# Performance work log

Measured on AMD Instinct MI355X. Metric: run time of the kernel, lower is better.

The kernel has to match this reference:

```python
import jax, jax.numpy as jnp
import numpy as np

B = 32768
IN_DIM = 768
HIDDENS = [2048, 1024, 512]
EMBED_DIM = 128
NUM_EMB = 1024
DEPTH = 3


def setup_inputs() -> dict:
    key = jax.random.key(0)
    ks = jax.random.split(key, 20)
    d = {"x": jax.random.normal(ks[0], (B, IN_DIM), dtype=jnp.float32)}
    # Encoder: in -> h0 -> h1 -> h2 -> embed  (weights stored as [in, out])
    enc_dims = [IN_DIM] + HIDDENS + [EMBED_DIM]
    for i in range(4):
        fan_in = enc_dims[i]
        d[f"enc_W{i+1}"] = jax.random.normal(ks[1 + i], (enc_dims[i], enc_dims[i + 1]), dtype=jnp.float32) / np.sqrt(fan_in)
        d[f"enc_b{i+1}"] = jnp.zeros((enc_dims[i + 1],), dtype=jnp.float32)
    # Decoder: embed -> h0 -> h1 -> h2 -> in
    dec_dims = [EMBED_DIM] + HIDDENS + [IN_DIM]
    for i in range(4):
        fan_in = dec_dims[i]
        d[f"dec_W{i+1}"] = jax.random.normal(ks[5 + i], (dec_dims[i], dec_dims[i + 1]), dtype=jnp.float32) / np.sqrt(fan_in)
        d[f"dec_b{i+1}"] = jnp.zeros((dec_dims[i + 1],), dtype=jnp.float32)
    # Codebook (nn.Embedding weight, initialized ~ N(0,1) as in the module)
    d["codebook"] = jax.random.normal(ks[9], (NUM_EMB, EMBED_DIM), dtype=jnp.float32)
    return d


def _encoder(x, W1, b1, W2, b2, W3, b3, W4, b4):
    x = jax.nn.relu(x @ W1 + b1)
    x = jax.nn.relu(x @ W2 + b2)
    x = jax.nn.relu(x @ W3 + b3)
    return x @ W4 + b4


def _decoder(x, W1, b1, W2, b2, W3, b3, W4, b4):
    x = jax.nn.relu(x @ W1 + b1)
    x = jax.nn.relu(x @ W2 + b2)
    x = jax.nn.relu(x @ W3 + b3)
    return x @ W4 + b4


def reference(x,
              enc_W1, enc_b1, enc_W2, enc_b2, enc_W3, enc_b3, enc_W4, enc_b4,
              dec_W1, dec_b1, dec_W2, dec_b2, dec_W3, dec_b3, dec_W4, dec_b4,
              codebook):
    z = _encoder(x, enc_W1, enc_b1, enc_W2, enc_b2, enc_W3, enc_b3, enc_W4, enc_b4)
    z_det = jax.lax.stop_gradient(z)

    cb_sq = jnp.sum(codebook * codebook, axis=1)  # [K]
    residue = z_det
    z_hat = jnp.zeros_like(z_det)
    codes = []
    for _ in range(DEPTH):  # residual quantization loop
        # squared L2 distances [B, K]
        dist = (jnp.sum(residue * residue, axis=1, keepdims=True)
                + cb_sq
                - 2.0 * residue @ codebook.T)
        idx = jnp.argmin(dist, axis=1)          # [B]
        codes.append(idx)
        z_hat = z_hat + codebook[idx]           # gather codebook vectors
        residue = z_det - z_hat
    all_codes = jnp.stack(codes, axis=1)        # [B, DEPTH] int

    # straight-through estimator: forward uses z_hat, grad flows through z
    z_flow = z + jax.lax.stop_gradient(z_hat - z)
    x_recon = _decoder(z_flow, dec_W1, dec_b1, dec_W2, dec_b2, dec_W3, dec_b3, dec_W4, dec_b4)
    return (x_recon, all_codes)
```

## Files before the change

kernel.cpp:

```cpp
#include <hip/hip_runtime.h>

#define FLT_MAX_C 3.402823466e+38f

typedef __attribute__((ext_vector_type(8))) __bf16 bf16x8;
typedef __attribute__((ext_vector_type(4))) float f32x4;

static __device__ __forceinline__ ushort f2bf(float x) {
    union { float f; unsigned u; } v; v.f = x;
    unsigned r = (v.u + 0x7FFFu + ((v.u >> 16) & 1u)) >> 16;
    return (ushort)r;
}

static __device__ __forceinline__ void xcd_swz(int& bx, int& by) {
    const int gx = gridDim.x;
    const int nwg = gx * gridDim.y;
    const int bid = blockIdx.y * gx + blockIdx.x;
    const int q = nwg >> 3, r = nwg & 7;
    const int xcd = bid & 7, lid = bid >> 3;
    const int swz = (xcd < r ? xcd * (q + 1) : r * (q + 1) + (xcd - r) * q) + lid;
    bx = swz % gx;
    by = swz / gx;
}

template<bool RELU>
__device__ __forceinline__ void gemm_f32_dev(
    const float* __restrict__ A, const float* __restrict__ W,
    const float* __restrict__ bias, float* __restrict__ C, int K, int N,
    int bxi, int byi)
{
    __shared__ float As[8][128];
    __shared__ float Bs[8][132];
    const int tid = threadIdx.x;
    const int bm = byi << 7;
    const int bn = bxi << 7;

    const int la_row = tid >> 1;
    const int la_k   = (tid & 1) << 2;
    const int lb_row = tid >> 5;
    const int lb_col = (tid & 31) << 2;
    const int tm4 = (tid >> 4) << 2;
    const int tn4 = (tid & 15) << 2;

    float acc[8][8];
    #pragma unroll
    for (int i = 0; i < 8; ++i)
        #pragma unroll
        for (int j = 0; j < 8; ++j) acc[i][j] = 0.f;

    const float* aptr = A + (size_t)(bm + la_row) * K + la_k;
    const float* bptr = W + (size_t)lb_row * N + bn + lb_col;

    float4 av = *(const float4*)(aptr);
    float4 bv = *(const float4*)(bptr);

    for (int k0 = 0; k0 < K; k0 += 8) {
        __syncthreads();
        As[la_k + 0][la_row] = av.x;
        As[la_k + 1][la_row] = av.y;
        As[la_k + 2][la_row] = av.z;
        As[la_k + 3][la_row] = av.w;
        *(float4*)(&Bs[lb_row][lb_col]) = bv;
        __syncthreads();
        if (k0 + 8 < K) {
            av = *(const float4*)(aptr + k0 + 8);
            bv = *(const float4*)(bptr + (size_t)(k0 + 8) * N);
        }
        #pragma unroll
        for (int kk = 0; kk < 8; ++kk) {
            float a[8], b[8];
            *(float4*)(a)     = *(const float4*)(&As[kk][tm4]);
            *(float4*)(a + 4) = *(const float4*)(&As[kk][tm4 + 64]);
            *(float4*)(b)     = *(const float4*)(&Bs[kk][tn4]);
            *(float4*)(b + 4) = *(const float4*)(&Bs[kk][tn4 + 64]);
            #pragma unroll
            for (int i = 0; i < 8; ++i)
                #pragma unroll
                for (int j = 0; j < 8; ++j)
                    acc[i][j] = fmaf(a[i], b[j], acc[i][j]);
        }
    }

    float bv0[8];
    #pragma unroll
    for (int j = 0; j < 8; ++j)
        bv0[j] = bias[bn + tn4 + (j < 4 ? j : 60 + j)];

    #pragma unroll
    for (int i = 0; i < 8; ++i) {
        int row = bm + tm4 + (i < 4 ? i : 60 + i);
        float* cp = C + (size_t)row * N + bn + tn4;
        float4 v0, v1;
        v0.x = acc[i][0] + bv0[0]; v0.y = acc[i][1] + bv0[1];
        v0.z = acc[i][2] + bv0[2]; v0.w = acc[i][3] + bv0[3];
        v1.x = acc[i][4] + bv0[4]; v1.y = acc[i][5] + bv0[5];
        v1.z = acc[i][6] + bv0[6]; v1.w = acc[i][7] + bv0[7];
        if (RELU) {
            v0.x = fmaxf(v0.x, 0.f); v0.y = fmaxf(v0.y, 0.f);
            v0.z = fmaxf(v0.z, 0.f); v0.w = fmaxf(v0.w, 0.f);
            v1.x = fmaxf(v1.x, 0.f); v1.y = fmaxf(v1.y, 0.f);
            v1.z = fmaxf(v1.z, 0.f); v1.w = fmaxf(v1.w, 0.f);
        }
        *(float4*)(cp) = v0;
        *(float4*)(cp + 64) = v1;
    }
}

template<bool RELU>
__device__ __forceinline__ void gemm_f32_wide_dev(
    const float* __restrict__ A, const float* __restrict__ W,
    const float* __restrict__ bias, float* __restrict__ C, int K, int N,
    int bxi, int byi, void* smem)
{
    float (*As)[128] = (float(*)[128])smem;
    float (*Bs)[260] = (float(*)[260])((char*)smem + 4096);
    const int tid = threadIdx.x;
    const int bm = byi << 7;
    const int bn = bxi << 8;

    const int la_row = tid >> 1;
    const int la_k   = (tid & 1) << 2;
    const int tm4 = (tid >> 4) << 2;
    const int tn4 = (tid & 15) << 2;
    const int bf_row  = tid >> 6;
    const int bf_col4 = (tid & 63) << 2;

    float acc[8][16];
    #pragma unroll
    for (int i = 0; i < 8; ++i)
        #pragma unroll
        for (int j = 0; j < 16; ++j) acc[i][j] = 0.f;

    const float* aptr = A + (size_t)(bm + la_row) * K + la_k;
    const float* bptr = W + (size_t)bf_row * N + bn + bf_col4;

    float4 av = *(const float4*)(aptr);
    float4 bv0 = *(const float4*)(bptr);
    float4 bv1 = *(const float4*)(bptr + (size_t)4 * N);

    for (int k0 = 0; k0 < K; k0 += 8) {
        __syncthreads();
        As[la_k + 0][la_row] = av.x;
        As[la_k + 1][la_row] = av.y;
        As[la_k + 2][la_row] = av.z;
        As[la_k + 3][la_row] = av.w;
        *(float4*)(&Bs[bf_row][bf_col4])     = bv0;
        *(float4*)(&Bs[bf_row + 4][bf_col4]) = bv1;
        __syncthreads();
        if (k0 + 8 < K) {
            av  = *(const float4*)(aptr + k0 + 8);
            bv0 = *(const float4*)(bptr + (size_t)(k0 + 8) * N);
            bv1 = *(const float4*)(bptr + (size_t)(k0 + 12) * N);
        }
        #pragma unroll
        for (int kk = 0; kk < 8; ++kk) {
            float a[8], b[16];
            *(float4*)(a)      = *(const float4*)(&As[kk][tm4]);
            *(float4*)(a + 4)  = *(const float4*)(&As[kk][tm4 + 64]);
            #pragma unroll
            for (int q = 0; q < 4; ++q)
                *(float4*)(b + q * 4) = *(const float4*)(&Bs[kk][tn4 + 64 * q]);
            #pragma unroll
            for (int i = 0; i < 8; ++i)
                #pragma unroll
                for (int j = 0; j < 16; ++j)
                    acc[i][j] = fmaf(a[i], b[j], acc[i][j]);
        }
    }

    float bb[16];
    #pragma unroll
    for (int q = 0; q < 4; ++q)
        #pragma unroll
        for (int jj = 0; jj < 4; ++jj)
            bb[q * 4 + jj] = bias[bn + tn4 + 64 * q + jj];

    #pragma unroll
    for (int i = 0; i < 8; ++i) {
        int row = bm + tm4 + (i < 4 ? i : 60 + i);
        float* cp = C + (size_t)row * N + bn + tn4;
        #pragma unroll
        for (int q = 0; q < 4; ++q) {
            float4 v;
            v.x = acc[i][q * 4 + 0] + bb[q * 4 + 0];
            v.y = acc[i][q * 4 + 1] + bb[q * 4 + 1];
            v.z = acc[i][q * 4 + 2] + bb[q * 4 + 2];
            v.w = acc[i][q * 4 + 3] + bb[q * 4 + 3];
            if (RELU) {
                v.x = fmaxf(v.x, 0.f); v.y = fmaxf(v.y, 0.f);
                v.z = fmaxf(v.z, 0.f); v.w = fmaxf(v.w, 0.f);
            }
            *(float4*)(cp + 64 * q) = v;
        }
    }
}

template<bool RELU>
__device__ __forceinline__ void gemm_f32_64_dev(
    const float* __restrict__ A, const float* __restrict__ W,
    const float* __restrict__ bias, float* __restrict__ C, int K, int N,
    int bxi, int byi)
{
    __shared__ float As[16][64];
    __shared__ float Bs[16][132];
    const int tid = threadIdx.x;
    const int bm = byi << 6;
    const int bn = bxi << 7;

    const int la_row = tid & 63;
    const int la_k   = (tid >> 6) << 2;
    const int lb_row = tid >> 5;
    const int lb_col = (tid & 31) << 2;
    const int tr = tid >> 4;
    const int tc = tid & 15;

    float acc[4][8];
    #pragma unroll
    for (int i = 0; i < 4; ++i)
        #pragma unroll
        for (int j = 0; j < 8; ++j) acc[i][j] = 0.f;

    const float* aptr = A + (size_t)(bm + la_row) * K + la_k;
    const float* bptr = W + (size_t)lb_row * N + bn + lb_col;

    float4 av = *(const float4*)(aptr);
    float4 bv0 = *(const float4*)(bptr);
    float4 bv1 = *(const float4*)(bptr + (size_t)8 * N);

    for (int k0 = 0; k0 < K; k0 += 16) {
        __syncthreads();
        As[la_k + 0][la_row] = av.x;
        As[la_k + 1][la_row] = av.y;
        As[la_k + 2][la_row] = av.z;
        As[la_k + 3][la_row] = av.w;
        *(float4*)(&Bs[lb_row][lb_col]) = bv0;
        *(float4*)(&Bs[lb_row + 8][lb_col]) = bv1;
        __syncthreads();
        if (k0 + 16 < K) {
            av  = *(const float4*)(aptr + k0 + 16);
            bv0 = *(const float4*)(bptr + (size_t)(k0 + 16) * N);
            bv1 = *(const float4*)(bptr + (size_t)(k0 + 24) * N);
        }
        #pragma unroll
        for (int kk = 0; kk < 16; ++kk) {
            float a[4], b[8];
            *(float4*)(a) = *(const float4*)(&As[kk][tr << 2]);
            *(float4*)(b)     = *(const float4*)(&Bs[kk][tc << 2]);
            *(float4*)(b + 4) = *(const float4*)(&Bs[kk][(tc << 2) + 64]);
            #pragma unroll
            for (int i = 0; i < 4; ++i)
                #pragma unroll
                for (int j = 0; j < 8; ++j)
                    acc[i][j] = fmaf(a[i], b[j], acc[i][j]);
        }
    }

    float bb[8];
    #pragma unroll
    for (int j = 0; j < 8; ++j)
        bb[j] = bias[bn + (tc << 2) + (j < 4 ? j : 60 + j)];

    #pragma unroll
    for (int i = 0; i < 4; ++i) {
        float* cp = C + (size_t)(bm + (tr << 2) + i) * N + bn + (tc << 2);
        float4 v0, v1;
        v0.x = acc[i][0] + bb[0]; v0.y = acc[i][1] + bb[1];
        v0.z = acc[i][2] + bb[2]; v0.w = acc[i][3] + bb[3];
        v1.x = acc[i][4] + bb[4]; v1.y = acc[i][5] + bb[5];
        v1.z = acc[i][6] + bb[6]; v1.w = acc[i][7] + bb[7];
        if (RELU) {
            v0.x = fmaxf(v0.x, 0.f); v0.y = fmaxf(v0.y, 0.f);
            v0.z = fmaxf(v0.z, 0.f); v0.w = fmaxf(v0.w, 0.f);
            v1.x = fmaxf(v1.x, 0.f); v1.y = fmaxf(v1.y, 0.f);
            v1.z = fmaxf(v1.z, 0.f); v1.w = fmaxf(v1.w, 0.f);
        }
        *(float4*)(cp) = v0;
        *(float4*)(cp + 64) = v1;
    }
}

template<bool RELU, bool OUTF32>
__device__ __forceinline__ void gemm_bf16_dev(
    const ushort* __restrict__ A, const ushort* __restrict__ Wt,
    const float* __restrict__ bias, void* __restrict__ C, int K, int N,
    int bxi, int byi)
{
    __shared__ __align__(16) ushort As[128][64];
    __shared__ __align__(16) ushort Bs[128][64];
    const int tid  = threadIdx.x;
    const int lane = tid & 63;
    const int wv   = tid >> 6;
    const int wm   = (wv >> 1) << 6;
    const int wn   = (wv & 1) << 6;
    const int bm   = byi << 7;
    const int bn   = bxi << 7;
    const int lr   = lane & 15;
    const int lh   = lane >> 4;

    f32x4 acc[4][4];
    #pragma unroll
    for (int m = 0; m < 4; ++m)
        #pragma unroll
        for (int n = 0; n < 4; ++n) acc[m][n] = (f32x4){0.f, 0.f, 0.f, 0.f};

    for (int k0 = 0; k0 < K; k0 += 64) {
        __syncthreads();
        #pragma unroll
        for (int i = 0; i < 4; ++i) {
            const int c    = wv * 4 + i;
            const int boff = c * 1024 + lane * 16;
            const int r    = boff >> 7;
            const int cbt  = boff & 127;
            const char* sa = (const char*)A  + (((size_t)(bm + r) * K + k0) << 1) + cbt;
            const char* sb = (const char*)Wt + (((size_t)(bn + r) * K + k0) << 1) + cbt;
            __builtin_amdgcn_global_load_lds((const void*)sa, (void*)(&As[0][0] + c * 512), 16, 0, 0);
            __builtin_amdgcn_global_load_lds((const void*)sb, (void*)(&Bs[0][0] + c * 512), 16, 0, 0);
        }
        __syncthreads();
        #pragma unroll
        for (int kk = 0; kk < 64; kk += 32) {
            bf16x8 af[4], bfr[4];
            #pragma unroll
            for (int m = 0; m < 4; ++m)
                af[m] = *(const bf16x8*)&As[wm + m * 16 + lr][kk + lh * 8];
            #pragma unroll
            for (int n = 0; n < 4; ++n)
                bfr[n] = *(const bf16x8*)&Bs[wn + n * 16 + lr][kk + lh * 8];
            #pragma unroll
            for (int m = 0; m < 4; ++m)
                #pragma unroll
                for (int n = 0; n < 4; ++n)
                    acc[m][n] = __builtin_amdgcn_mfma_f32_16x16x32_bf16(
                        af[m], bfr[n], acc[m][n], 0, 0, 0);
        }
    }

    #pragma unroll
    for (int n = 0; n < 4; ++n) {
        const int col = bn + wn + n * 16 + lr;
        const float bcol = bias[col];
        #pragma unroll
        for (int m = 0; m < 4; ++m) {
            #pragma unroll
            for (int i = 0; i < 4; ++i) {
                const int row = bm + wm + m * 16 + lh * 4 + i;
                float v = acc[m][n][i] + bcol;
                if (RELU) v = fmaxf(v, 0.f);
                if (OUTF32) ((float*)C)[(size_t)row * N + col] = v;
                else        ((ushort*)C)[(size_t)row * N + col] = f2bf(v);
            }
        }
    }
}

__device__ __forceinline__ void wt_convert_dev(
    const float* __restrict__ W, ushort* __restrict__ Wt, int K, int N,
    int bx, int by, void* smem)
{
    ushort (*t)[65] = (ushort(*)[65])smem;
    const int kb = by << 6, nb = bx << 6;
    const int c  = threadIdx.x & 63;
    const int r0 = (threadIdx.x >> 6) << 4;
    #pragma unroll
    for (int i = 0; i < 16; ++i)
        t[r0 + i][c] = f2bf(W[(size_t)(kb + r0 + i) * N + nb + c]);
    __syncthreads();
    #pragma unroll
    for (int i = 0; i < 16; ++i)
        Wt[(size_t)(nb + r0 + i) * K + kb + c] = t[c][r0 + i];
}

__device__ __forceinline__ void prep_dispatch(
    int b,
    const float* dW1, const float* dW2, const float* dW3, const float* dW4,
    ushort* Wt1, ushort* Wt2, ushort* Wt3, ushort* Wt4,
    const float* cb, float* sq, float* cbt, void* smem)
{
    if (b < 64)  { wt_convert_dev(dW1, Wt1, 128,  2048, b % 32, b / 32, smem); return; }
    b -= 64;
    if (b < 512) { wt_convert_dev(dW2, Wt2, 2048, 1024, b % 16, b / 16, smem); return; }
    b -= 512;
    if (b < 128) { wt_convert_dev(dW3, Wt3, 1024, 512,  b % 8,  b / 8,  smem); return; }
    b -= 128;
    if (b < 96)  { wt_convert_dev(dW4, Wt4, 512,  768,  b % 12, b / 12, smem); return; }
    b -= 96;
    if (b < 4) {
        int k = b * 256 + threadIdx.x;
        const float* r = cb + ((size_t)k << 7);
        float s = 0.f;
        #pragma unroll 8
        for (int d = 0; d < 128; ++d) s = fmaf(r[d], r[d], s);
        sq[k] = s;
        return;
    }
    b -= 4;
    {
        float (*t)[65] = (float(*)[65])smem;
        const int kb = (b % 16) << 6;
        const int db = (b / 16) << 6;
        const int c  = threadIdx.x & 63;
        const int r0 = (threadIdx.x >> 6) << 4;
        #pragma unroll
        for (int i = 0; i < 16; ++i)
            t[r0 + i][c] = cb[(size_t)(kb + r0 + i) * 128 + db + c];
        __syncthreads();
        #pragma unroll
        for (int i = 0; i < 16; ++i)
            cbt[(size_t)(db + r0 + i) * 1024 + kb + c] = t[c][r0 + i];
    }
}

__global__ __launch_bounds__(256) void enc1_prep(
    const float* A, const float* W, const float* b, float* C, int encb,
    const float* dW1, const float* dW2, const float* dW3, const float* dW4,
    ushort* Wt1, ushort* Wt2, ushort* Wt3, ushort* Wt4,
    const float* cb, float* sq, float* cbt)
{
    __shared__ __align__(16) char pool[16640];
    const int bid = blockIdx.x;
    if (bid < encb) {
        gemm_f32_wide_dev<true>(A, W, b, C, 768, 2048, bid & 7, bid >> 3, pool);
    } else {
        prep_dispatch(bid - encb, dW1, dW2, dW3, dW4, Wt1, Wt2, Wt3, Wt4,
                      cb, sq, cbt, pool);
    }
}

__global__ __launch_bounds__(256) void enc2_gemm(const float* A, const float* W, const float* b, float* C)
{ __shared__ __align__(16) char pool[12416];
  int bx, by; xcd_swz(bx, by);
  gemm_f32_wide_dev<true>(A, W, b, C, 2048, 1024, bx, by, pool); }
__global__ __launch_bounds__(256) void enc3_gemm(const float* A, const float* W, const float* b, float* C)
{ int bx, by; xcd_swz(bx, by); gemm_f32_dev<true>(A, W, b, C, 1024, 512, bx, by); }
__global__ __launch_bounds__(256) void enc4_gemm(const float* A, const float* W, const float* b, float* C)
{ int bx, by; xcd_swz(bx, by); gemm_f32_64_dev<false>(A, W, b, C, 512, 128, bx, by); }
__global__ __launch_bounds__(256) void dec1_gemm(const ushort* A, const ushort* Wt, const float* b, void* C)
{ int bx, by; xcd_swz(bx, by); gemm_bf16_dev<true, false>(A, Wt, b, C, 128, 2048, bx, by); }
__global__ __launch_bounds__(256) void dec2_gemm(const ushort* A, const ushort* Wt, const float* b, void* C)
{ int bx, by; xcd_swz(bx, by); gemm_bf16_dev<true, false>(A, Wt, b, C, 2048, 1024, bx, by); }
__global__ __launch_bounds__(256) void dec3_gemm(const ushort* A, const ushort* Wt, const float* b, void* C)
{ int bx, by; xcd_swz(bx, by); gemm_bf16_dev<true, false>(A, Wt, b, C, 1024, 512, bx, by); }
__global__ __launch_bounds__(256) void dec4_gemm(const ushort* A, const ushort* Wt, const float* b, void* C)
{ int bx, by; xcd_swz(bx, by); gemm_bf16_dev<false, true>(A, Wt, b, C, 512, 768, bx, by); }

__global__ __launch_bounds__(256) void rq_all(
    const float* __restrict__ z, const float* __restrict__ cbt,
    const float* __restrict__ sq, const float* __restrict__ cb,
    ushort* __restrict__ ZHb, float* __restrict__ codes)
{
    __shared__ float As[128][68];
    __shared__ float Bs[32][132];
    __shared__ float sqs[1024];
    __shared__ float rrs[64];

    const int tid = threadIdx.x;
    const int bm  = blockIdx.x << 6;
    const int tr  = tid >> 4;
    const int c   = tid & 15;
    const int tn4 = c << 2;
    const int lb_row = tid >> 5;
    const int lb_col = (tid & 31) << 2;

    #pragma unroll
    for (int i = 0; i < 4; ++i) sqs[tid + (i << 8)] = sq[tid + (i << 8)];

    float zh[4][8];
    #pragma unroll
    for (int i = 0; i < 4; ++i) {
        const int r_  = (tr << 2) + i;
        const float* zp = z + (size_t)(bm + r_) * 128 + (c << 3);
        float4 z0 = *(const float4*)(zp);
        float4 z1 = *(const float4*)(zp + 4);
        #pragma unroll
        for (int j = 0; j < 8; ++j) zh[i][j] = 0.f;
        As[(c << 3) + 0][r_] = z0.x; As[(c << 3) + 1][r_] = z0.y;
        As[(c << 3) + 2][r_] = z0.z; As[(c << 3) + 3][r_] = z0.w;
        As[(c << 3) + 4][r_] = z1.x; As[(c << 3) + 5][r_] = z1.y;
        As[(c << 3) + 6][r_] = z1.z; As[(c << 3) + 7][r_] = z1.w;
        float p = z0.x * z0.x;
        p = fmaf(z0.y, z0.y, p); p = fmaf(z0.z, z0.z, p);
        p = fmaf(z0.w, z0.w, p); p = fmaf(z1.x, z1.x, p);
        p = fmaf(z1.y, z1.y, p); p = fmaf(z1.z, z1.z, p);
        p = fmaf(z1.w, z1.w, p);
        #pragma unroll
        for (int o = 8; o >= 1; o >>= 1) p += __shfl_xor(p, o);
        if (c == 0) rrs[r_] = p;
    }
    __syncthreads();

    for (int t = 0; t < 3; ++t) {
        float rr_[4];
        #pragma unroll
        for (int i = 0; i < 4; ++i) rr_[i] = rrs[(tr << 2) + i];

        float best_d[4] = {FLT_MAX_C, FLT_MAX_C, FLT_MAX_C, FLT_MAX_C};
        int   best_i[4] = {0, 0, 0, 0};

        for (int bx = 0; bx < 8; ++bx) {
            const int bn = bx << 7;
            const float* bptr = cbt + (size_t)lb_row * 1024 + bn + lb_col;
            float4 bv0 = *(const float4*)(bptr);
            float4 bv1 = *(const float4*)(bptr + (size_t)8  * 1024);
            float4 bv2 = *(const float4*)(bptr + (size_t)16 * 1024);
            float4 bv3 = *(const float4*)(bptr + (size_t)24 * 1024);

            float acc[4][8];
            #pragma unroll
            for (int i = 0; i < 4; ++i)
                #pragma unroll
                for (int j = 0; j < 8; ++j) acc[i][j] = 0.f;

            for (int k0 = 0; k0 < 128; k0 += 32) {
                __syncthreads();
                *(float4*)(&Bs[lb_row +  0][lb_col]) = bv0;
                *(float4*)(&Bs[lb_row +  8][lb_col]) = bv1;
                *(float4*)(&Bs[lb_row + 16][lb_col]) = bv2;
                *(float4*)(&Bs[lb_row + 24][lb_col]) = bv3;
                __syncthreads();
                if (k0 + 32 < 128) {
                    bv0 = *(const float4*)(bptr + (size_t)(k0 + 32) * 1024);
                    bv1 = *(const float4*)(bptr + (size_t)(k0 + 40) * 1024);
                    bv2 = *(const float4*)(bptr + (size_t)(k0 + 48) * 1024);
                    bv3 = *(const float4*)(bptr + (size_t)(k0 + 56) * 1024);
                }
                #pragma unroll
                for (int kk = 0; kk < 32; ++kk) {
                    float a[4], b[8];
                    *(float4*)(a)     = *(const float4*)(&As[k0 + kk][tr << 2]);
                    *(float4*)(b)     = *(const float4*)(&Bs[kk][tn4]);
                    *(float4*)(b + 4) = *(const float4*)(&Bs[kk][tn4 + 64]);
                    #pragma unroll
                    for (int i = 0; i < 4; ++i)
                        #pragma unroll
                        for (int j = 0; j < 8; ++j)
                            acc[i][j] = fmaf(a[i], b[j], acc[i][j]);
                }
            }
            #pragma unroll
            for (int i = 0; i < 4; ++i) {
                #pragma unroll
                for (int j = 0; j < 8; ++j) {
                    const int col = bn + tn4 + (j < 4 ? j : 60 + j);
                    float d = (rr_[i] + sqs[col]) - 2.f * acc[i][j];
                    if (d < best_d[i]) { best_d[i] = d; best_i[i] = col; }
                }
            }
        }

        #pragma unroll
        for (int i = 0; i < 4; ++i) {
            float bd = best_d[i]; int bi = best_i[i];
            #pragma unroll
            for (int o = 8; o >= 1; o >>= 1) {
                float od = __shfl_xor(bd, o);
                int   oi = __shfl_xor(bi, o);
                if (od < bd || (od == bd && oi < bi)) { bd = od; bi = oi; }
            }
            best_i[i] = bi;
        }

        __syncthreads();

        #pragma unroll
        for (int i = 0; i < 4; ++i) {
            const int r_  = (tr << 2) + i;
            const int row = bm + r_;
            if (c == 0) codes[(size_t)row * 3 + t] = (float)best_i[i];

            const float* cbp = cb + ((size_t)best_i[i] << 7) + (c << 3);
            float4 c0 = *(const float4*)(cbp);
            float4 c1 = *(const float4*)(cbp + 4);
            zh[i][0] += c0.x; zh[i][1] += c0.y;
            zh[i][2] += c0.z; zh[i][3] += c0.w;
            zh[i][4] += c1.x; zh[i][5] += c1.y;
            zh[i][6] += c1.z; zh[i][7] += c1.w;

            if (t < 2) {
                const float* zp = z + (size_t)row * 128 + (c << 3);
                float4 z0 = *(const float4*)(zp);
                float4 z1 = *(const float4*)(zp + 4);
                float r0 = z0.x - zh[i][0], r1 = z0.y - zh[i][1];
                float r2 = z0.z - zh[i][2], r3 = z0.w - zh[i][3];
                float r4 = z1.x - zh[i][4], r5 = z1.y - zh[i][5];
                float r6 = z1.z - zh[i][6], r7 = z1.w - zh[i][7];
                As[(c << 3) + 0][r_] = r0; As[(c << 3) + 1][r_] = r1;
                As[(c << 3) + 2][r_] = r2; As[(c << 3) + 3][r_] = r3;
                As[(c << 3) + 4][r_] = r4; As[(c << 3) + 5][r_] = r5;
                As[(c << 3) + 6][r_] = r6; As[(c << 3) + 7][r_] = r7;
                float p = r0 * r0;
                p = fmaf(r1, r1, p); p = fmaf(r2, r2, p);
                p = fmaf(r3, r3, p); p = fmaf(r4, r4, p);
                p = fmaf(r5, r5, p); p = fmaf(r6, r6, p);
                p = fmaf(r7, r7, p);
                #pragma unroll
                for (int o = 8; o >= 1; o >>= 1) p += __shfl_xor(p, o);
                if (c == 0) rrs[r_] = p;
            } else {
                ushort4 o0, o1;
                o0.x = f2bf(zh[i][0]); o0.y = f2bf(zh[i][1]);
                o0.z = f2bf(zh[i][2]); o0.w = f2bf(zh[i][3]);
                o1.x = f2bf(zh[i][4]); o1.y = f2bf(zh[i][5]);
                o1.z = f2bf(zh[i][6]); o1.w = f2bf(zh[i][7]);
                ushort* zbp = ZHb + (size_t)row * 128 + (c << 3);
                *(ushort4*)(zbp)     = o0;
                *(ushort4*)(zbp + 4) = o1;
            }
        }
        if (t < 2) __syncthreads();
    }
}

extern "C" void kernel_launch(void* const* d_in, const int* in_sizes, int n_in,
                              void* d_out, int out_size, void* d_ws, size_t ws_size,
                              hipStream_t stream)
{
    const float* x   = (const float*)d_in[0];
    const float* eW1 = (const float*)d_in[1];
    const float* eb1 = (const float*)d_in[2];
    const float* eW2 = (const float*)d_in[3];
    const float* eb2 = (const float*)d_in[4];
    const float* eW3 = (const float*)d_in[5];
    const float* eb3 = (const float*)d_in[6];
    const float* eW4 = (const float*)d_in[7];
    const float* eb4 = (const float*)d_in[8];
    const float* dW1 = (const float*)d_in[9];
    const float* db1 = (const float*)d_in[10];
    const float* dW2 = (const float*)d_in[11];
    const float* db2 = (const float*)d_in[12];
    const float* dW3 = (const float*)d_in[13];
    const float* db3 = (const float*)d_in[14];
    const float* dW4 = (const float*)d_in[15];
    const float* db4 = (const float*)d_in[16];
    const float* cb  = (const float*)d_in[17];

    float* out   = (float*)d_out;
    float* codes = out + (size_t)32768 * 768;

    ushort* Wt1 = (ushort*)d_ws;
    ushort* Wt2 = Wt1 + (size_t)2048 * 128;
    ushort* Wt3 = Wt2 + (size_t)1024 * 2048;
    ushort* Wt4 = Wt3 + (size_t)512 * 1024;
    float*  sq  = (float*)(Wt4 + (size_t)768 * 512);
    float*  cbt = sq + 1024;
    float*  act = cbt + (size_t)128 * 1024;
    const size_t fixed_b = (char*)act - (char*)d_ws;

    int mc = 32768;
    while (mc > 1024) {
        if (fixed_b + (size_t)mc * 15104 <= ws_size) break;
        mc >>= 1;
    }

    float*  R1  = act;
    float*  R2  = R1 + (size_t)mc * 2048;
    float*  R3  = R2 + (size_t)mc * 1024;
    float*  RZ  = R3 + (size_t)mc * 512;
    ushort* ZHb = (ushort*)(RZ + (size_t)mc * 128);
    ushort* D1  = (ushort*)R1;
    ushort* D2  = (ushort*)R2;
    ushort* D3  = (ushort*)R3;

    const int mg = mc >> 7;
    bool first = true;
    for (int r0 = 0; r0 < 32768; r0 += mc) {
        const float* xi     = x     + (size_t)r0 * 768;
        float*       outi   = out   + (size_t)r0 * 768;
        float*       codesi = codes + (size_t)r0 * 3;
        const int encb = 8 * mg;
        const int prepb = first ? 836 : 0;
        enc1_prep<<<encb + prepb, 256, 0, stream>>>(
            xi, eW1, eb1, R1, encb,
            dW1, dW2, dW3, dW4, Wt1, Wt2, Wt3, Wt4, cb, sq, cbt);
        first = false;
        enc2_gemm<<<dim3( 4, mg), 256, 0, stream>>>(R1, eW2, eb2, R2);
        enc3_gemm<<<dim3( 4, mg), 256, 0, stream>>>(R2, eW3, eb3, R3);
        enc4_gemm<<<dim3( 1, mc >> 6), 256, 0, stream>>>(R3, eW4, eb4, RZ);
        rq_all<<<mc >> 6, 256, 0, stream>>>(RZ, cbt, sq, cb, ZHb, codesi);
        dec1_gemm<<<dim3(16, mg), 256, 0, stream>>>(ZHb, Wt1, db1, D1);
        dec2_gemm<<<dim3( 8, mg), 256, 0, stream>>>(D1,  Wt2, db2, D2);
        dec3_gemm<<<dim3( 4, mg), 256, 0, stream>>>(D2,  Wt3, db3, D3);
        dec4_gemm<<<dim3( 6, mg), 256, 0, stream>>>(D3,  Wt4, db4, outi);
    }
}
```

Measured before the change: 3.779 ms.

## Double-buffer LDS tiles in bf16 GEMM with K-step of 32

```diff
diff --git a/kernel.cpp b/kernel.cpp
--- a/kernel.cpp
+++ b/kernel.cpp
@@ -284,8 +284,8 @@
     const float* __restrict__ bias, void* __restrict__ C, int K, int N,
     int bxi, int byi)
 {
-    __shared__ __align__(16) ushort As[128][64];
-    __shared__ __align__(16) ushort Bs[128][64];
+    __shared__ __align__(16) ushort As[2][128][32];
+    __shared__ __align__(16) ushort Bs[2][128][32];
     const int tid  = threadIdx.x;
     const int lane = tid & 63;
     const int wv   = tid >> 6;
@@ -302,36 +302,44 @@
         #pragma unroll
         for (int n = 0; n < 4; ++n) acc[m][n] = (f32x4){0.f, 0.f, 0.f, 0.f};
 
-    for (int k0 = 0; k0 < K; k0 += 64) {
-        __syncthreads();
-        #pragma unroll
-        for (int i = 0; i < 4; ++i) {
-            const int c    = wv * 4 + i;
-            const int boff = c * 1024 + lane * 16;
-            const int r    = boff >> 7;
-            const int cbt  = boff & 127;
-            const char* sa = (const char*)A  + (((size_t)(bm + r) * K + k0) << 1) + cbt;
-            const char* sb = (const char*)Wt + (((size_t)(bn + r) * K + k0) << 1) + cbt;
-            __builtin_amdgcn_global_load_lds((const void*)sa, (void*)(&As[0][0] + c * 512), 16, 0, 0);
-            __builtin_amdgcn_global_load_lds((const void*)sb, (void*)(&Bs[0][0] + c * 512), 16, 0, 0);
-        }
-        __syncthreads();
-        #pragma unroll
-        for (int kk = 0; kk < 64; kk += 32) {
-            bf16x8 af[4], bfr[4];
-            #pragma unroll
-            for (int m = 0; m < 4; ++m)
-                af[m] = *(const bf16x8*)&As[wm + m * 16 + lr][kk + lh * 8];
+    auto stage = [&](int t, int bsel) {
+        const int k0 = t << 5;
+        #pragma unroll
+        for (int i = 0; i < 2; ++i) {
+            const int blk = i * 4 + wv;
+            const int f   = blk * 64 + lane;
+            const int r   = f >> 2;
+            const int cbyte = (f & 3) << 4;
+            const char* sa = (const char*)A  + (((size_t)(bm + r) * K + k0) << 1) + cbyte;
+            const char* sb = (const char*)Wt + (((size_t)(bn + r) * K + k0) << 1) + cbyte;
+            __builtin_amdgcn_global_load_lds((const void*)sa,
+                (void*)((char*)(&As[bsel][0][0]) + blk * 1024), 16, 0, 0);
+            __builtin_amdgcn_global_load_lds((const void*)sb,
+                (void*)((char*)(&Bs[bsel][0][0]) + blk * 1024), 16, 0, 0);
+        }
+    };
+
+    const int nt = K >> 5;
+    stage(0, 0);
+    __syncthreads();
+
+    for (int t = 0; t < nt; ++t) {
+        const int b = t & 1;
+        if (t + 1 < nt) stage(t + 1, b ^ 1);
+        bf16x8 af[4], bfr[4];
+        #pragma unroll
+        for (int m = 0; m < 4; ++m)
+            af[m] = *(const bf16x8*)&As[b][wm + m * 16 + lr][lh * 8];
+        #pragma unroll
+        for (int n = 0; n < 4; ++n)
+            bfr[n] = *(const bf16x8*)&Bs[b][wn + n * 16 + lr][lh * 8];
+        #pragma unroll
+        for (int m = 0; m < 4; ++m)
             #pragma unroll
             for (int n = 0; n < 4; ++n)
-                bfr[n] = *(const bf16x8*)&Bs[wn + n * 16 + lr][kk + lh * 8];
-            #pragma unroll
-            for (int m = 0; m < 4; ++m)
-                #pragma unroll
-                for (int n = 0; n < 4; ++n)
-                    acc[m][n] = __builtin_amdgcn_mfma_f32_16x16x32_bf16(
-                        af[m], bfr[n], acc[m][n], 0, 0, 0);
-        }
+                acc[m][n] = __builtin_amdgcn_mfma_f32_16x16x32_bf16(
+                    af[m], bfr[n], acc[m][n], 0, 0, 0);
+        __syncthreads();
     }
 
     #pragma unroll
```

New measurement: 3.763 ms. Within noise of the previous version (-0.4%).
